# Performance work log

Hardware: AMD Instinct MI355X
Metric: run time of the kernel (lower is better)

## Reference

```python
import jax, jax.numpy as jnp
import numpy as np

K = 20          # neighbors
BN_EPS = 1e-5


def _knn_idx(x, k):
    """x: [B, C, N] -> idx of k nearest neighbors [B, N, k] (by squared distance, self included)."""
    xx = jnp.sum(x * x, axis=1)                       # [B, N]
    inner = jnp.einsum('bcn,bcm->bnm', x, x)          # [B, N, N]
    neg_sqdist = 2.0 * inner - xx[:, :, None] - xx[:, None, :]
    return jax.lax.top_k(neg_sqdist, k)[1]            # [B, N, k]


def _graph_feature(x, k):
    """x: [B, C, N] -> edge features cat(x_j - x_i, x_i): [B, 2C, N, k]."""
    idx = _knn_idx(x, k)                              # [B, N, k]
    xT = x.transpose(0, 2, 1)                         # [B, N, C]
    nbrs = jax.vmap(lambda xt, ii: xt[ii])(xT, idx)   # [B, N, k, C] gather
    center = xT[:, :, None, :]                        # [B, N, 1, C]
    feat = jnp.concatenate(
        [nbrs - center, jnp.broadcast_to(center, nbrs.shape)], axis=-1)  # [B, N, k, 2C]
    return feat.transpose(0, 3, 1, 2)                 # [B, 2C, N, k]


def _conv_bn_lrelu(feat, W, gamma, beta, mean, var):
    """1x1 Conv2d (no bias) + BatchNorm (given stats) + LeakyReLU(0.2). feat: [B, Cin, N, k]."""
    y = jnp.einsum('oc,bcnk->bonk', W, feat)
    scale = (gamma / jnp.sqrt(var + BN_EPS))[None, :, None, None]
    y = (y - mean[None, :, None, None]) * scale + beta[None, :, None, None]
    return jnp.where(y > 0, y, 0.2 * y)


def setup_inputs() -> dict:
    key = jax.random.key(0)
    ks = list(jax.random.split(key, 32))
    B, N = 8, 1024
    f32 = jnp.float32

    def w(kk, o, i):
        return jax.random.normal(kk, (o, i), dtype=f32) / np.sqrt(i)

    def bn(k1, k2, k3, k4, c):
        g = jax.random.uniform(k1, (c,), dtype=f32, minval=0.5, maxval=1.5)
        b = jax.random.normal(k2, (c,), dtype=f32) * 0.05
        m = jax.random.normal(k3, (c,), dtype=f32) * 0.05
        v = jax.random.uniform(k4, (c,), dtype=f32, minval=0.5, maxval=1.5)
        return g, b, m, v

    x = jax.random.normal(ks[0], (B, N, 3), dtype=f32)
    W0 = w(ks[1], 64, 6);    g0, b0, m0, v0 = bn(ks[2], ks[3], ks[4], ks[5], 64)
    W1 = w(ks[6], 128, 128); g1, b1, m1, v1 = bn(ks[7], ks[8], ks[9], ks[10], 128)
    W2 = w(ks[11], 256, 256); g2, b2, m2, v2 = bn(ks[12], ks[13], ks[14], ks[15], 256)
    Wf = w(ks[16], 512, 896); gf, bf, mf, vf = bn(ks[17], ks[18], ks[19], ks[20], 512)
    We = w(ks[21], 256, 512)
    return dict(x=x,
                W0=W0, g0=g0, b0=b0, m0=m0, v0=v0,
                W1=W1, g1=g1, b1=b1, m1=m1, v1=v1,
                W2=W2, g2=g2, b2=b2, m2=m2, v2=v2,
                Wf=Wf, gf=gf, bf=bf, mf=mf, vf=vf,
                We=We)


def reference(x, W0, g0, b0, m0, v0, W1, g1, b1, m1, v1,
              W2, g2, b2, m2, v2, Wf, gf, bf, mf, vf, We):
    h = x.transpose(0, 2, 1)                          # [B, 3, N]
    outs = []
    for (W, g, b, m, v) in ((W0, g0, b0, m0, v0),
                            (W1, g1, b1, m1, v1),
                            (W2, g2, b2, m2, v2)):
        gfeat = _graph_feature(h, K)                  # [B, 2C, N, k]
        y = _conv_bn_lrelu(gfeat, W, g, b, m, v)      # [B, Cout, N, k]
        h = y.mean(axis=-1)                           # max-free EdgeConv pool over k
        outs.append(h)
    cat = jnp.concatenate(outs, axis=1)               # [B, 448, N]
    gfeat = _graph_feature(cat, K)                    # [B, 896, N, k]
    y = _conv_bn_lrelu(gfeat, Wf, gf, bf, mf, vf)     # [B, 512, N, k]
    pooled = y.mean(axis=-1).mean(axis=-1)            # [B, 512] (pool over k then N)
    return pooled @ We.T                              # [B, num_features]
```

## Files before the change

### kernel.cpp

```cpp
#include <hip/hip_runtime.h>
#include <cstdint>

#define KNN 20
#define BV 8
#define NV 1024

template <int CTRL>
__device__ __forceinline__ unsigned dppmax(unsigned x) {
    unsigned m = (unsigned)__builtin_amdgcn_update_dpp((int)x, (int)x, CTRL, 0xf, 0xf, false);
    return (x > m) ? x : m;
}
template <int CTRL>
__device__ __forceinline__ unsigned dppmin(unsigned x) {
    unsigned m = (unsigned)__builtin_amdgcn_update_dpp((int)x, (int)x, CTRL, 0xf, 0xf, false);
    return (x < m) ? x : m;
}
__device__ __forceinline__ unsigned wave_max_u32(unsigned x) {
    x = dppmax<0xB1>(x); x = dppmax<0x4E>(x); x = dppmax<0x141>(x);
    x = dppmax<0x140>(x); x = dppmax<0x142>(x); x = dppmax<0x143>(x);
    return (unsigned)__builtin_amdgcn_readlane((int)x, 63);
}
__device__ __forceinline__ unsigned wave_min_u32(unsigned x) {
    x = dppmin<0xB1>(x); x = dppmin<0x4E>(x); x = dppmin<0x141>(x);
    x = dppmin<0x140>(x); x = dppmin<0x142>(x); x = dppmin<0x143>(x);
    return (unsigned)__builtin_amdgcn_readlane((int)x, 63);
}

__global__ __launch_bounds__(256) void k_transpose(const float* __restrict__ x, float* __restrict__ hx) {
    int id = blockIdx.x * 256 + threadIdx.x;
    if (id >= BV * 3 * NV) return;
    int n = id % NV;
    int c = (id / NV) % 3;
    int b = id / (3 * NV);
    hx[id] = x[(b * NV + n) * 3 + c];
}

__global__ __launch_bounds__(256) void k_xx(const float* __restrict__ h, float* __restrict__ xx,
                                            int C, int bstride) {
    int id = blockIdx.x * 256 + threadIdx.x;
    int n = id % NV, b = id / NV;
    if (b >= BV) return;
    const float* hp = h + (size_t)b * bstride + n;
    float s = 0.f;
    for (int c = 0; c < C; ++c) { float v = hp[(size_t)c * NV]; s += v * v; }
    xx[b * NV + n] = s;
}

__global__ __launch_bounds__(512, 8) void k_knn(const float* __restrict__ h, const float* __restrict__ xx,
                                                int C, int bstride,
                                                unsigned* __restrict__ sval, int* __restrict__ sidx) {
    __shared__ float Bs[8][256];
    __shared__ float As[8][32];
    const int bx = blockIdx.x;
    const int tile = bx >> 5, panel = bx & 31;
    const int b = panel & 7, quarter = panel >> 3;
    const int i0 = tile * 32, jbase = quarter * 256;
    const int t = threadIdx.x, lane = t & 63, w = t >> 6;
    const int irow = i0 + w * 4;
    float acc[4][4] = {};
    const float* hb = h + (size_t)b * bstride;

    for (int c0 = 0; c0 < C; c0 += 8) {
        __syncthreads();
        {
            int cc = t >> 6, g = t & 63;
            float4 v = make_float4(0.f, 0.f, 0.f, 0.f);
            if (c0 + cc < C) v = *(const float4*)&hb[(size_t)(c0 + cc) * NV + jbase + g * 4];
            *(float4*)&Bs[cc][g * 4] = v;
        }
        if (t < 64) {
#pragma unroll
            for (int r = 0; r < 4; ++r) {
                int e = r * 64 + t;
                int cc = e >> 5, ii = e & 31;
                As[cc][ii] = (c0 + cc < C) ? hb[(size_t)(c0 + cc) * NV + i0 + ii] : 0.f;
            }
        }
        __syncthreads();
#pragma unroll
        for (int c = 0; c < 8; ++c) {
            float4 arv = *(const float4*)&As[c][w * 4];
            float ar[4] = {arv.x, arv.y, arv.z, arv.w};
            float4 bv = *(const float4*)&Bs[c][lane * 4];
            float br[4] = {bv.x, bv.y, bv.z, bv.w};
#pragma unroll
            for (int a = 0; a < 4; ++a)
#pragma unroll
                for (int q = 0; q < 4; ++q) acc[a][q] += ar[a] * br[q];
        }
    }

    const float* xb = xx + b * NV;
    float4 xv = *(const float4*)&xb[jbase + lane * 4];
    float xxj[4] = {xv.x, xv.y, xv.z, xv.w};
#pragma unroll
    for (int a = 0; a < 4; ++a) {
        float xi = xb[irow + a];
#pragma unroll
        for (int q = 0; q < 4; ++q) acc[a][q] = 2.f * acc[a][q] - xi - xxj[q];
    }

#pragma unroll 1
    for (int s = 0; s < KNN; ++s) {
#pragma unroll
        for (int a = 0; a < 4; ++a) {
            bool g0 = acc[a][1] > acc[a][0];
            float v0 = g0 ? acc[a][1] : acc[a][0]; int q0 = g0 ? 1 : 0;
            bool g1 = acc[a][3] > acc[a][2];
            float v1 = g1 ? acc[a][3] : acc[a][2]; int q1 = g1 ? 3 : 2;
            bool gf = v1 > v0;
            float bv = gf ? v1 : v0;
            int bq = gf ? q1 : q0;

            unsigned u = __float_as_uint(bv);
            unsigned su = ((int)u < 0) ? ~u : (u | 0x80000000u);
            int myj = jbase + (lane << 2) + bq;
            unsigned gmax = wave_max_u32(su);
            unsigned cand = (su == gmax) ? (unsigned)myj : 0xFFFFFFFFu;
            int j = (int)wave_min_u32(cand);
            if (lane == 0) {
                size_t o = ((size_t)(b * NV + irow + a) * 4 + quarter) * KNN + s;
                sval[o] = gmax;
                sidx[o] = j;
            }
            int wq = (myj == j) ? bq : 9;
#pragma unroll
            for (int q = 0; q < 4; ++q)
                if (wq == q) acc[a][q] = -3.4e38f;
        }
    }
}

__global__ __launch_bounds__(256) void k_merge(const unsigned* __restrict__ sval,
                                               const int* __restrict__ sidx,
                                               int* __restrict__ idx) {
    int row = blockIdx.x * 256 + threadIdx.x;
    if (row >= BV * NV) return;
    const unsigned* v = sval + (size_t)row * 4 * KNN;
    const int* ii = sidx + (size_t)row * 4 * KNN;
    int pos[4] = {0, 0, 0, 0};
    unsigned hv[4]; int hj[4];
#pragma unroll
    for (int l = 0; l < 4; ++l) { hv[l] = v[l * KNN]; hj[l] = ii[l * KNN]; }
    int* op = idx + (size_t)row * KNN;
#pragma unroll 1
    for (int s = 0; s < KNN; ++s) {
        bool b01 = (hv[1] > hv[0]) || (hv[1] == hv[0] && hj[1] < hj[0]);
        unsigned v01 = b01 ? hv[1] : hv[0]; int j01 = b01 ? hj[1] : hj[0]; int l01 = b01 ? 1 : 0;
        bool b23 = (hv[3] > hv[2]) || (hv[3] == hv[2] && hj[3] < hj[2]);
        unsigned v23 = b23 ? hv[3] : hv[2]; int j23 = b23 ? hj[3] : hj[2]; int l23 = b23 ? 3 : 2;
        bool bf = (v23 > v01) || (v23 == v01 && j23 < j01);
        int win = bf ? l23 : l01;
        op[s] = bf ? j23 : j01;
#pragma unroll
        for (int l = 0; l < 4; ++l) {
            if (win == l) {
                int np = pos[l] + 1; pos[l] = np;
                bool ok = np < KNN;
                hv[l] = ok ? v[l * KNN + np] : 0u;
                hj[l] = ok ? ii[l * KNN + np] : 0x7FFFFFFF;
            }
        }
    }
}

__global__ __launch_bounds__(256) void k_pack(const float* __restrict__ W, float* __restrict__ wb,
                                              int C, int O) {
    int id = blockIdx.x * 256 + threadIdx.x;
    if (id >= 2 * O * C) return;
    int c = id % C, o = (id / C) % O, half = id / (C * O);
    float wl = W[(size_t)o * 2 * C + c];
    wb[id] = half ? (W[(size_t)o * 2 * C + C + c] - wl) : wl;
}

__global__ __launch_bounds__(256) void k_gemm(const float* __restrict__ A, int astride,
                                              const float* __restrict__ h, int bstride, int C,
                                              float* __restrict__ out, int O) {
    __shared__ float Ws[8][64], Hs[8][128];
    const int b = blockIdx.x, n0 = blockIdx.y * 128, o0 = blockIdx.z * 64;
    const int t = threadIdx.x, tx = t & 15, ty = t >> 4;
    float acc[4][8] = {};
    const float* hb = h + (size_t)b * bstride;
    for (int c0 = 0; c0 < C; c0 += 8) {
#pragma unroll
        for (int q = 0; q < 2; ++q) {
            int e = t + q * 256;
            int oo = e >> 3, cc = e & 7;
            Ws[cc][oo] = ((c0 + cc) < C) ? A[(size_t)(o0 + oo) * astride + c0 + cc] : 0.f;
        }
        {
            int cc = t >> 5, nn4 = t & 31;
            float4 v = make_float4(0.f, 0.f, 0.f, 0.f);
            if (c0 + cc < C) v = *(const float4*)&hb[(size_t)(c0 + cc) * NV + n0 + nn4 * 4];
            *(float4*)&Hs[cc][nn4 * 4] = v;
        }
        __syncthreads();
#pragma unroll
        for (int c = 0; c < 8; ++c) {
            float4 wv = *(const float4*)&Ws[c][ty * 4];
            float ar[4] = {wv.x, wv.y, wv.z, wv.w};
            float br[8];
            float4 h0 = *(const float4*)&Hs[c][tx * 4];
            float4 h1 = *(const float4*)&Hs[c][64 + tx * 4];
            br[0] = h0.x; br[1] = h0.y; br[2] = h0.z; br[3] = h0.w;
            br[4] = h1.x; br[5] = h1.y; br[6] = h1.z; br[7] = h1.w;
#pragma unroll
            for (int a = 0; a < 4; ++a)
#pragma unroll
                for (int q = 0; q < 8; ++q) acc[a][q] += ar[a] * br[q];
        }
        __syncthreads();
    }
#pragma unroll
    for (int a = 0; a < 4; ++a) {
        int o = o0 + ty * 4 + a;
        float* outp = out + ((size_t)b * O + o) * NV + n0;
        float4 s0 = make_float4(acc[a][0], acc[a][1], acc[a][2], acc[a][3]);
        float4 s1 = make_float4(acc[a][4], acc[a][5], acc[a][6], acc[a][7]);
        *(float4*)&outp[tx * 4] = s0;
        *(float4*)&outp[64 + tx * 4] = s1;
    }
}

__global__ __launch_bounds__(256) void k_edge(const float* __restrict__ pd,
                                              const int* __restrict__ idx,
                                              const float* __restrict__ ga, const float* __restrict__ be,
                                              const float* __restrict__ mu, const float* __restrict__ va,
                                              float* __restrict__ out, int out_bstride, int O) {
    const int b = blockIdx.x;
    const int n = blockIdx.y * 256 + threadIdx.x;
    const int o0 = blockIdx.z * 4;
    const int* ip = idx + ((size_t)b * NV + n) * KNN;
    int jj[KNN];
#pragma unroll
    for (int k = 0; k < KNN; ++k) jj[k] = ip[k];
#pragma unroll
    for (int a = 0; a < 4; ++a) {
        const int o = o0 + a;
        const float al = ga[o] / sqrtf(va[o] + 1e-5f);
        const float c0 = be[o] - mu[o] * al;
        const float* pb = pd + ((size_t)b * 2 * O + o) * NV;
        const float dv  = pd[((size_t)b * 2 * O + O + o) * NV + n];
        float s = 0.f;
#pragma unroll
        for (int k = 0; k < KNN; ++k) {
            float y = fmaf(al, pb[jj[k]] + dv, c0);
            s += (y > 0.f) ? y : 0.2f * y;
        }
        out[(size_t)b * out_bstride + (size_t)o * NV + n] = s * (1.f / KNN);
    }
}

__global__ __launch_bounds__(256) void k_pool(const float* __restrict__ hf, float* __restrict__ pooled) {
    const int o = blockIdx.x, b = blockIdx.y;
    const float* hp = hf + ((size_t)b * 512 + o) * NV;
    float s = 0.f;
    for (int i = threadIdx.x; i < NV; i += 256) s += hp[i];
#pragma unroll
    for (int off = 32; off > 0; off >>= 1) s += __shfl_down(s, off, 64);
    __shared__ float red[4];
    if ((threadIdx.x & 63) == 0) red[threadIdx.x >> 6] = s;
    __syncthreads();
    if (threadIdx.x == 0)
        pooled[(size_t)b * 512 + o] = (red[0] + red[1] + red[2] + red[3]) * (1.f / NV);
}

__global__ __launch_bounds__(256) void k_final(const float* __restrict__ pooled, const float* __restrict__ We,
                                               float* __restrict__ out) {
    const int j = threadIdx.x, b = blockIdx.x;
    __shared__ float ps[512];
    for (int o = threadIdx.x; o < 512; o += 256) ps[o] = pooled[b * 512 + o];
    __syncthreads();
    float s = 0.f;
    for (int o = 0; o < 512; ++o) s += ps[o] * We[(size_t)j * 512 + o];
    out[b * 256 + j] = s;
}

extern "C" void kernel_launch(void* const* d_in, const int* in_sizes, int n_in,
                              void* d_out, int out_size, void* d_ws, size_t ws_size,
                              hipStream_t stream) {
    const float* x  = (const float*)d_in[0];
    const float* W0 = (const float*)d_in[1];
    const float* g0 = (const float*)d_in[2];
    const float* b0 = (const float*)d_in[3];
    const float* m0 = (const float*)d_in[4];
    const float* v0 = (const float*)d_in[5];
    const float* W1 = (const float*)d_in[6];
    const float* g1 = (const float*)d_in[7];
    const float* b1 = (const float*)d_in[8];
    const float* m1 = (const float*)d_in[9];
    const float* v1 = (const float*)d_in[10];
    const float* W2 = (const float*)d_in[11];
    const float* g2 = (const float*)d_in[12];
    const float* b2 = (const float*)d_in[13];
    const float* m2 = (const float*)d_in[14];
    const float* v2 = (const float*)d_in[15];
    const float* Wf = (const float*)d_in[16];
    const float* gf = (const float*)d_in[17];
    const float* bf = (const float*)d_in[18];
    const float* mf = (const float*)d_in[19];
    const float* vf = (const float*)d_in[20];
    const float* We = (const float*)d_in[21];

    float* ws = (float*)d_ws;
    float* hx     = ws;
    float* cat    = hx + 24576;
    float* xx     = cat + 3670016;
    int*   idx    = (int*)(xx + 8192);
    float* pd     = (float*)(idx + 163840);
    float* wb     = pd + 8388608;
    float* hf     = wb + 458752;
    float* pooled = hf + 4194304;
    unsigned* sval = (unsigned*)(pooled + 4096);
    int*      sidx = (int*)(sval + 655360);

    k_transpose<<<96, 256, 0, stream>>>(x, hx);

    auto run_layer = [&](const float* h, int C, int bstride, const float* W,
                         const float* g, const float* be, const float* m, const float* v,
                         int O, float* outp, int obstride) {
        k_xx<<<32, 256, 0, stream>>>(h, xx, C, bstride);
        k_knn<<<1024, 512, 0, stream>>>(h, xx, C, bstride, sval, sidx);
        k_merge<<<32, 256, 0, stream>>>(sval, sidx, idx);
        int pn = 2 * O * C;
        k_pack<<<(pn + 255) / 256, 256, 0, stream>>>(W, wb, C, O);
        k_gemm<<<dim3(8, 8, 2 * O / 64), 256, 0, stream>>>(wb, C, h, bstride, C, pd, 2 * O);
        k_edge<<<dim3(8, 4, O / 4), 256, 0, stream>>>(pd, idx, g, be, m, v, outp, obstride, O);
    };

    run_layer(hx, 3, 3 * NV, W0, g0, b0, m0, v0, 64, cat, 448 * NV);
    run_layer(cat, 64, 448 * NV, W1, g1, b1, m1, v1, 128, cat + 64 * NV, 448 * NV);
    run_layer(cat + 64 * NV, 128, 448 * NV, W2, g2, b2, m2, v2, 256, cat + 192 * NV, 448 * NV);
    run_layer(cat, 448, 448 * NV, Wf, gf, bf, mf, vf, 512, hf, 512 * NV);

    k_pool<<<dim3(512, 8), 256, 0, stream>>>(hf, pooled);
    k_final<<<8, 256, 0, stream>>>(pooled, We, (float*)d_out);
}
```

Baseline: 935.4 us.

## Double kNN row tile per wave and replace argmin reduction with ballot

The kNN kernel now gives each wave 8 query rows instead of 4, covering 64 rows per block with half as many blocks. The A tile is loaded with float4 reads, so each B element loaded from LDS is reused across more rows. The tie-break that used a second wave-wide min reduction is replaced by a ballot, find-first-set and readlane, which cuts the cross-lane work in each top-k step. The cost is higher register pressure (launch bounds occupancy hint lowered from 8 to 4) and fewer blocks to spread across the GPU.

```diff
diff --git a/kernel.cpp b/kernel.cpp
--- a/kernel.cpp
+++ b/kernel.cpp
@@ -10,19 +10,9 @@
     unsigned m = (unsigned)__builtin_amdgcn_update_dpp((int)x, (int)x, CTRL, 0xf, 0xf, false);
     return (x > m) ? x : m;
 }
-template <int CTRL>
-__device__ __forceinline__ unsigned dppmin(unsigned x) {
-    unsigned m = (unsigned)__builtin_amdgcn_update_dpp((int)x, (int)x, CTRL, 0xf, 0xf, false);
-    return (x < m) ? x : m;
-}
 __device__ __forceinline__ unsigned wave_max_u32(unsigned x) {
     x = dppmax<0xB1>(x); x = dppmax<0x4E>(x); x = dppmax<0x141>(x);
     x = dppmax<0x140>(x); x = dppmax<0x142>(x); x = dppmax<0x143>(x);
-    return (unsigned)__builtin_amdgcn_readlane((int)x, 63);
-}
-__device__ __forceinline__ unsigned wave_min_u32(unsigned x) {
-    x = dppmin<0xB1>(x); x = dppmin<0x4E>(x); x = dppmin<0x141>(x);
-    x = dppmin<0x140>(x); x = dppmin<0x142>(x); x = dppmin<0x143>(x);
     return (unsigned)__builtin_amdgcn_readlane((int)x, 63);
 }
 
@@ -46,18 +36,18 @@
     xx[b * NV + n] = s;
 }
 
-__global__ __launch_bounds__(512, 8) void k_knn(const float* __restrict__ h, const float* __restrict__ xx,
+__global__ __launch_bounds__(512, 4) void k_knn(const float* __restrict__ h, const float* __restrict__ xx,
                                                 int C, int bstride,
                                                 unsigned* __restrict__ sval, int* __restrict__ sidx) {
     __shared__ float Bs[8][256];
-    __shared__ float As[8][32];
+    __shared__ float As[8][64];
     const int bx = blockIdx.x;
     const int tile = bx >> 5, panel = bx & 31;
     const int b = panel & 7, quarter = panel >> 3;
-    const int i0 = tile * 32, jbase = quarter * 256;
+    const int i0 = tile * 64, jbase = quarter * 256;
     const int t = threadIdx.x, lane = t & 63, w = t >> 6;
-    const int irow = i0 + w * 4;
-    float acc[4][4] = {};
+    const int irow = i0 + w * 8;
+    float acc[8][4] = {};
     const float* hb = h + (size_t)b * bstride;
 
     for (int c0 = 0; c0 < C; c0 += 8) {
@@ -68,23 +58,22 @@
             if (c0 + cc < C) v = *(const float4*)&hb[(size_t)(c0 + cc) * NV + jbase + g * 4];
             *(float4*)&Bs[cc][g * 4] = v;
         }
-        if (t < 64) {
-#pragma unroll
-            for (int r = 0; r < 4; ++r) {
-                int e = r * 64 + t;
-                int cc = e >> 5, ii = e & 31;
-                As[cc][ii] = (c0 + cc < C) ? hb[(size_t)(c0 + cc) * NV + i0 + ii] : 0.f;
-            }
+        if (t < 128) {
+            int cc = t >> 4, ii = (t & 15) * 4;
+            float4 v = make_float4(0.f, 0.f, 0.f, 0.f);
+            if (c0 + cc < C) v = *(const float4*)&hb[(size_t)(c0 + cc) * NV + i0 + ii];
+            *(float4*)&As[cc][ii] = v;
         }
         __syncthreads();
 #pragma unroll
         for (int c = 0; c < 8; ++c) {
-            float4 arv = *(const float4*)&As[c][w * 4];
-            float ar[4] = {arv.x, arv.y, arv.z, arv.w};
+            float4 a0 = *(const float4*)&As[c][w * 8];
+            float4 a1 = *(const float4*)&As[c][w * 8 + 4];
+            float ar[8] = {a0.x, a0.y, a0.z, a0.w, a1.x, a1.y, a1.z, a1.w};
             float4 bv = *(const float4*)&Bs[c][lane * 4];
             float br[4] = {bv.x, bv.y, bv.z, bv.w};
 #pragma unroll
-            for (int a = 0; a < 4; ++a)
+            for (int a = 0; a < 8; ++a)
 #pragma unroll
                 for (int q = 0; q < 4; ++q) acc[a][q] += ar[a] * br[q];
         }
@@ -94,7 +83,7 @@
     float4 xv = *(const float4*)&xb[jbase + lane * 4];
     float xxj[4] = {xv.x, xv.y, xv.z, xv.w};
 #pragma unroll
-    for (int a = 0; a < 4; ++a) {
+    for (int a = 0; a < 8; ++a) {
         float xi = xb[irow + a];
 #pragma unroll
         for (int q = 0; q < 4; ++q) acc[a][q] = 2.f * acc[a][q] - xi - xxj[q];
@@ -103,7 +92,7 @@
 #pragma unroll 1
     for (int s = 0; s < KNN; ++s) {
 #pragma unroll
-        for (int a = 0; a < 4; ++a) {
+        for (int a = 0; a < 8; ++a) {
             bool g0 = acc[a][1] > acc[a][0];
             float v0 = g0 ? acc[a][1] : acc[a][0]; int q0 = g0 ? 1 : 0;
             bool g1 = acc[a][3] > acc[a][2];
@@ -114,16 +103,17 @@
 
             unsigned u = __float_as_uint(bv);
             unsigned su = ((int)u < 0) ? ~u : (u | 0x80000000u);
+            unsigned gmax = wave_max_u32(su);
+            unsigned long long m = __ballot(su == gmax);
+            int wl = (int)__ffsll(m) - 1;
             int myj = jbase + (lane << 2) + bq;
-            unsigned gmax = wave_max_u32(su);
-            unsigned cand = (su == gmax) ? (unsigned)myj : 0xFFFFFFFFu;
-            int j = (int)wave_min_u32(cand);
+            int j = __builtin_amdgcn_readlane(myj, wl);
             if (lane == 0) {
                 size_t o = ((size_t)(b * NV + irow + a) * 4 + quarter) * KNN + s;
                 sval[o] = gmax;
                 sidx[o] = j;
             }
-            int wq = (myj == j) ? bq : 9;
+            int wq = (lane == wl) ? bq : 9;
 #pragma unroll
             for (int q = 0; q < 4; ++q)
                 if (wq == q) acc[a][q] = -3.4e38f;
@@ -320,7 +310,7 @@
                          const float* g, const float* be, const float* m, const float* v,
                          int O, float* outp, int obstride) {
         k_xx<<<32, 256, 0, stream>>>(h, xx, C, bstride);
-        k_knn<<<1024, 512, 0, stream>>>(h, xx, C, bstride, sval, sidx);
+        k_knn<<<512, 512, 0, stream>>>(h, xx, C, bstride, sval, sidx);
         k_merge<<<32, 256, 0, stream>>>(sval, sidx, idx);
         int pn = 2 * O * C;
         k_pack<<<(pn + 255) / 256, 256, 0, stream>>>(W, wb, C, O);
```

Measured after the change: 878.7 us. -6.1%, faster.
